# Kernel tuning notes

Hardware: AMD Instinct MI355X
Metric: run time of the kernel (lower is better)

## Reference

```python
import jax, jax.numpy as jnp
import numpy as np

# ---- static config (mirrors init_kwargs) ----
PILLAR_SIZE = 0.075
X_MIN, Y_MIN, Z_MIN = -54.0, -54.0, -5.0
X_MAX, Y_MAX, Z_MAX = 54.0, 54.0, 3.0
GRID_W = int(round((X_MAX - X_MIN) / PILLAR_SIZE))  # 1440
GRID_H = int(round((Y_MAX - Y_MIN) / PILLAR_SIZE))  # 1440
B = 4            # batch (lidar frames)
N = 800_000      # total points across batch
M = 120_000      # total occupied pillars across batch
C_IN = 5         # raw point features (x,y,z,intensity,timestamp)
C_GRP = 6 + C_IN # (xyz - pillar_center, xyz, pt_feature)
C_MLP = 32       # shared MLP output width
BN_EPS = 1e-3


def _pillar_centers(pillar_indices):
    """pillar_indices: (M,3) int [b, y, x] -> (M,3) float centers."""
    pi = pillar_indices.astype(jnp.float32)
    cx = (pi[:, 2] + 0.5) * PILLAR_SIZE + X_MIN
    cy = (pi[:, 1] + 0.5) * PILLAR_SIZE + Y_MIN
    cz = jnp.full_like(cx, 0.5 * (Z_MIN + Z_MAX))
    return jnp.stack([cx, cy, cz], axis=1)


def setup_inputs() -> dict:
    key = jax.random.key(0)
    ks = jax.random.split(key, 8)
    # occupied pillar cells [b, y, x]
    pil_b = jax.random.randint(ks[0], (M,), 0, B, dtype=jnp.int32)
    pil_y = jax.random.randint(ks[1], (M,), 0, GRID_H, dtype=jnp.int32)
    pil_x = jax.random.randint(ks[2], (M,), 0, GRID_W, dtype=jnp.int32)
    pillar_indices = jnp.stack([pil_b, pil_y, pil_x], axis=1)
    # each point belongs to exactly one pillar
    pillar_set_indices = jax.random.randint(ks[3], (N,), 0, M, dtype=jnp.int32)
    centers = _pillar_centers(pillar_indices)
    noise = jax.random.normal(ks[4], (N, 3), dtype=jnp.float32)
    noise = noise * jnp.array([0.3 * PILLAR_SIZE, 0.3 * PILLAR_SIZE, 1.5], jnp.float32)
    xyz = centers[pillar_set_indices] + noise  # points near their pillar center
    pt_feature = jax.random.normal(ks[5], (N, C_IN), dtype=jnp.float32)
    # shared MLP params: Linear(no bias) + BatchNorm1d(gamma, beta)
    W1 = jax.random.normal(ks[6], (C_GRP, C_MLP), dtype=jnp.float32) * np.float32(1.0 / np.sqrt(C_GRP))
    gamma1 = jnp.ones((C_MLP,), jnp.float32)
    beta1 = jnp.zeros((C_MLP,), jnp.float32)
    xyz_batch_cnt = jnp.full((B,), N // B, jnp.int32)
    return dict(xyz=xyz, pt_feature=pt_feature, W1=W1, gamma1=gamma1, beta1=beta1,
                pillar_indices=pillar_indices, pillar_set_indices=pillar_set_indices,
                xyz_batch_cnt=xyz_batch_cnt)


def reference(xyz, pt_feature, W1, gamma1, beta1, pillar_indices, pillar_set_indices, xyz_batch_cnt):
    # --- PillarQueryAndGroup: gather per-point grouped features ---
    centers = _pillar_centers(pillar_indices)            # (M, 3)
    ctr = centers[pillar_set_indices]                    # (N, 3) gather
    group_features = jnp.concatenate([xyz - ctr, xyz, pt_feature], axis=1)  # (N, 6+C)
    # --- shared MLP: Linear(no bias) -> BatchNorm1d (train-mode stats) -> ReLU ---
    h = group_features @ W1                              # (N, C_MLP)
    mean = jnp.mean(h, axis=0)
    var = jnp.var(h, axis=0)                             # biased, as torch BN uses for normalization
    h = (h - mean) * jax.lax.rsqrt(var + BN_EPS) * gamma1 + beta1
    h = jax.nn.relu(h)
    # --- scatter-max pool over pillars (CUDA scatter_max inits to 0) ---
    pooled = jax.ops.segment_max(h, pillar_set_indices, num_segments=M)
    pillar_features = jnp.maximum(pooled, 0.0)           # empty pillars -> 0; h >= 0 after ReLU
    return pillar_features                               # (M, C_MLP); dense features of SparseConvTensor
```

## Files before the change

kernel.cpp:

```cpp
#include <hip/hip_runtime.h>


#define CMLP 32
#define BN_EPS 1e-3f
#define PSIZE 0.075f
#define XMIN -54.0f
#define YMIN -54.0f
#define CZ   -1.0f
#define NREP 64
#define SCATB 4096

__device__ __forceinline__ unsigned enc_f(float x) {
  unsigned b = __float_as_uint(x);
  return (b & 0x80000000u) ? ~b : (b | 0x80000000u);
}
__device__ __forceinline__ float dec_f(unsigned u) {
  unsigned b = (u & 0x80000000u) ? (u & 0x7fffffffu) : ~u;
  return __uint_as_float(b);
}

__global__ void __launch_bounds__(256) scatter_stats_kernel(
    const float* __restrict__ xyz, const float* __restrict__ ptf,
    const float* __restrict__ W1, const float* __restrict__ gamma,
    const int* __restrict__ pil, const int* __restrict__ sidx,
    float* __restrict__ stats_rep, unsigned* __restrict__ outenc, int N) {
  const int tid = threadIdx.x;
  const int c = tid & 31;
  const float w0 = W1[0 * CMLP + c], w1 = W1[1 * CMLP + c];
  const float w2 = W1[2 * CMLP + c];
  const float wx = w0 + W1[3 * CMLP + c];
  const float wy = w1 + W1[4 * CMLP + c];
  const float wz = w2 + W1[5 * CMLP + c];
  const float nw0 = -w0, nw1 = -w1;
  const float c0 = -CZ * w2;
  const float w6 = W1[6 * CMLP + c], w7 = W1[7 * CMLP + c];
  const float w8 = W1[8 * CMLP + c], w9 = W1[9 * CMLP + c];
  const float w10 = W1[10 * CMLP + c];
  const float sgn = (gamma[c] < 0.f) ? -1.f : 1.f;
  float s = 0.f, ss = 0.f;
  const int hw0 = (blockIdx.x * 256 + tid) >> 5;
  const int nhw = (SCATB * 256) >> 5;
  int p = hw0;
  int m = (p < N) ? __builtin_nontemporal_load(&sidx[p]) : 0;
  while (p < N) {
    const int pn = p + nhw;
    const int mn = (pn < N) ? __builtin_nontemporal_load(&sidx[pn]) : 0;
    float cx = fmaf((float)pil[3 * m + 2] + 0.5f, PSIZE, XMIN);
    float cy = fmaf((float)pil[3 * m + 1] + 0.5f, PSIZE, YMIN);
    float x = __builtin_nontemporal_load(&xyz[3 * p]);
    float y = __builtin_nontemporal_load(&xyz[3 * p + 1]);
    float z = __builtin_nontemporal_load(&xyz[3 * p + 2]);
    float h = c0;
    h = fmaf(x, wx, h);
    h = fmaf(y, wy, h);
    h = fmaf(z, wz, h);
    h = fmaf(cx, nw0, h);
    h = fmaf(cy, nw1, h);
    h = fmaf(__builtin_nontemporal_load(&ptf[5 * p + 0]), w6, h);
    h = fmaf(__builtin_nontemporal_load(&ptf[5 * p + 1]), w7, h);
    h = fmaf(__builtin_nontemporal_load(&ptf[5 * p + 2]), w8, h);
    h = fmaf(__builtin_nontemporal_load(&ptf[5 * p + 3]), w9, h);
    h = fmaf(__builtin_nontemporal_load(&ptf[5 * p + 4]), w10, h);
    s += h;
    ss = fmaf(h, h, ss);
    atomicMax(&outenc[m * CMLP + c], enc_f(sgn * h));
    p = pn;
    m = mn;
  }
  s += __shfl_xor(s, 32);
  ss += __shfl_xor(ss, 32);
  __shared__ float red[4][64];
  const int wave = tid >> 6, lane = tid & 63;
  if (lane < 32) {
    red[wave][lane] = s;
    red[wave][32 + lane] = ss;
  }
  __syncthreads();
  if (tid < 64) {
    float v = red[0][tid] + red[1][tid] + red[2][tid] + red[3][tid];
    atomicAdd(&stats_rep[(blockIdx.x & (NREP - 1)) * 64 + tid], v);
  }
}

__global__ void finalize_kernel(const float* __restrict__ gamma,
                                const float* __restrict__ beta,
                                const float* __restrict__ stats_rep,
                                float* __restrict__ affine, float invN) {
  int c = threadIdx.x;
  if (c < CMLP) {
    float s = 0.f, ss = 0.f;
    for (int r = 0; r < NREP; r++) {
      s += stats_rep[r * 64 + c];
      ss += stats_rep[r * 64 + 32 + c];
    }
    float mean = s * invN;
    float var = ss * invN - mean * mean;
    float sc = gamma[c] * rsqrtf(var + BN_EPS);
    affine[c] = sc;
    affine[CMLP + c] = beta[c] - mean * sc;
  }
}

__global__ void __launch_bounds__(256) transform_kernel(
    unsigned* __restrict__ io, const float* __restrict__ affine, int total) {
  int i = blockIdx.x * 256 + threadIdx.x;
  if (i < total) {
    unsigned u = io[i];
    int c = i & 31;
    float v = 0.f;
    if (u) v = fmaxf(fmaf(fabsf(affine[c]), dec_f(u), affine[CMLP + c]), 0.f);
    io[i] = __float_as_uint(v);
  }
}

extern "C" void kernel_launch(void* const* d_in, const int* in_sizes, int n_in,
                              void* d_out, int out_size, void* d_ws, size_t ws_size,
                              hipStream_t stream) {
  const float* xyz = (const float*)d_in[0];
  const float* ptf = (const float*)d_in[1];
  const float* W1 = (const float*)d_in[2];
  const float* gamma = (const float*)d_in[3];
  const float* beta = (const float*)d_in[4];
  const int* pil = (const int*)d_in[5];
  const int* sidx = (const int*)d_in[6];
  unsigned* out = (unsigned*)d_out;

  int N = in_sizes[0] / 3;

  float* stats_rep = (float*)d_ws;
  float* affine = (float*)((char*)d_ws + NREP * 64 * sizeof(float));

  hipMemsetAsync(stats_rep, 0, NREP * 64 * sizeof(float), stream);
  hipMemsetAsync(out, 0, (size_t)out_size * sizeof(unsigned), stream);

  scatter_stats_kernel<<<SCATB, 256, 0, stream>>>(xyz, ptf, W1, gamma, pil,
                                                  sidx, stats_rep, out, N);
  finalize_kernel<<<1, 64, 0, stream>>>(gamma, beta, stats_rep, affine,
                                        1.0f / (float)N);
  transform_kernel<<<(out_size + 255) / 256, 256, 0, stream>>>(out, affine,
                                                               out_size);
}
```

Measured before the change: 189.3 us.

## Bucket points by pillar group and pool in shared memory instead of global atomics

Adds a counting-sort pipeline: a histogram of points per 32-pillar bucket, a prefix scan, and a scatter of point records into bucket order. A pool kernel then computes the MLP output per bucket and reduces the max with LDS atomics, writing each output tile once. This replaces scattered global atomicMax traffic and the output memset, at the cost of extra passes that write and re-read about 36 bytes per point through workspace. The fallback path, used when the workspace is too small, drops the nontemporal loads and adds a read-before-atomicMax check.

```diff
diff --git a/kernel.cpp b/kernel.cpp
--- a/kernel.cpp
+++ b/kernel.cpp
@@ -9,6 +9,9 @@
 #define CZ   -1.0f
 #define NREP 64
 #define SCATB 4096
+#define PPB 32
+#define HISTB 1024
+#define SCAT2B 2048
 
 __device__ __forceinline__ unsigned enc_f(float x) {
   unsigned b = __float_as_uint(x);
@@ -17,6 +20,136 @@
 __device__ __forceinline__ float dec_f(unsigned u) {
   unsigned b = (u & 0x80000000u) ? (u & 0x7fffffffu) : ~u;
   return __uint_as_float(b);
+}
+
+__global__ void __launch_bounds__(256) hist_kernel(
+    const int* __restrict__ sidx, int* __restrict__ hist, int N) {
+  const int stride = gridDim.x * 256;
+  for (int p = blockIdx.x * 256 + threadIdx.x; p < N; p += stride) {
+    int m = __builtin_nontemporal_load(&sidx[p]);
+    atomicAdd(&hist[m >> 5], 1);
+  }
+}
+
+__global__ void prefix_kernel(const int* __restrict__ hist,
+                              int* __restrict__ offs, int* __restrict__ cur,
+                              int nbkt) {
+  __shared__ int part[257];
+  const int t = threadIdx.x;
+  const int chunk = (nbkt + 255) >> 8;
+  const int lo = t * chunk;
+  const int hi = (lo + chunk < nbkt) ? lo + chunk : nbkt;
+  int s = 0;
+  for (int i = lo; i < hi; i++) s += hist[i];
+  part[t] = s;
+  __syncthreads();
+  if (t == 0) {
+    int acc = 0;
+    for (int i = 0; i < 256; i++) { int v = part[i]; part[i] = acc; acc += v; }
+    part[256] = acc;
+  }
+  __syncthreads();
+  int acc = part[t];
+  for (int i = lo; i < hi; i++) {
+    offs[i] = acc;
+    cur[i] = acc;
+    acc += hist[i];
+  }
+  if (t == 0) offs[nbkt] = part[256];
+}
+
+__global__ void __launch_bounds__(256) bucket_scatter_kernel(
+    const float* __restrict__ xyz, const float* __restrict__ ptf,
+    const int* __restrict__ sidx, int* __restrict__ cur,
+    float4* __restrict__ recA, float4* __restrict__ recB,
+    float* __restrict__ recC, int N) {
+  const int stride = gridDim.x * 256;
+  for (int p = blockIdx.x * 256 + threadIdx.x; p < N; p += stride) {
+    int m = __builtin_nontemporal_load(&sidx[p]);
+    float x = __builtin_nontemporal_load(&xyz[3 * p]);
+    float y = __builtin_nontemporal_load(&xyz[3 * p + 1]);
+    float z = __builtin_nontemporal_load(&xyz[3 * p + 2]);
+    float f0 = __builtin_nontemporal_load(&ptf[5 * p + 0]);
+    float f1 = __builtin_nontemporal_load(&ptf[5 * p + 1]);
+    float f2 = __builtin_nontemporal_load(&ptf[5 * p + 2]);
+    float f3 = __builtin_nontemporal_load(&ptf[5 * p + 3]);
+    float f4 = __builtin_nontemporal_load(&ptf[5 * p + 4]);
+    int idx = atomicAdd(&cur[m >> 5], 1);
+    recA[idx] = make_float4(x, y, z, __int_as_float(m));
+    recB[idx] = make_float4(f0, f1, f2, f3);
+    recC[idx] = f4;
+  }
+}
+
+__global__ void __launch_bounds__(256) pool_kernel(
+    const float4* __restrict__ recA, const float4* __restrict__ recB,
+    const float* __restrict__ recC, const int* __restrict__ offs,
+    const float* __restrict__ W1, const float* __restrict__ gamma,
+    const int* __restrict__ pil, float* __restrict__ stats_rep,
+    unsigned* __restrict__ outenc, int M) {
+  __shared__ unsigned lmax[PPB * CMLP];
+  const int tid = threadIdx.x;
+  const int c = tid & 31;
+  for (int i = tid; i < PPB * CMLP; i += 256) lmax[i] = 0u;
+  const float w0 = W1[0 * CMLP + c], w1 = W1[1 * CMLP + c];
+  const float w2 = W1[2 * CMLP + c];
+  const float wx = w0 + W1[3 * CMLP + c];
+  const float wy = w1 + W1[4 * CMLP + c];
+  const float wz = w2 + W1[5 * CMLP + c];
+  const float nw0 = -w0, nw1 = -w1;
+  const float c0 = -CZ * w2;
+  const float w6 = W1[6 * CMLP + c], w7 = W1[7 * CMLP + c];
+  const float w8 = W1[8 * CMLP + c], w9 = W1[9 * CMLP + c];
+  const float w10 = W1[10 * CMLP + c];
+  const float sgn = (gamma[c] < 0.f) ? -1.f : 1.f;
+  const int b = blockIdx.x;
+  const int base = offs[b], end = offs[b + 1];
+  const int p0 = b * PPB;
+  float s = 0.f, ss = 0.f;
+  __syncthreads();
+  for (int i = base + (tid >> 5); i < end; i += 8) {
+    float4 a = recA[i];
+    float4 f = recB[i];
+    float f4 = recC[i];
+    int m = __float_as_int(a.w);
+    float cx = fmaf((float)pil[3 * m + 2] + 0.5f, PSIZE, XMIN);
+    float cy = fmaf((float)pil[3 * m + 1] + 0.5f, PSIZE, YMIN);
+    float h = c0;
+    h = fmaf(a.x, wx, h);
+    h = fmaf(a.y, wy, h);
+    h = fmaf(a.z, wz, h);
+    h = fmaf(cx, nw0, h);
+    h = fmaf(cy, nw1, h);
+    h = fmaf(f.x, w6, h);
+    h = fmaf(f.y, w7, h);
+    h = fmaf(f.z, w8, h);
+    h = fmaf(f.w, w9, h);
+    h = fmaf(f4, w10, h);
+    s += h;
+    ss = fmaf(h, h, ss);
+    atomicMax(&lmax[((m - p0) << 5) | c], enc_f(sgn * h));
+  }
+  __syncthreads();
+  const int gbase = b * (PPB * CMLP);
+  const int glim = M * CMLP;
+#pragma unroll
+  for (int k = 0; k < 4; k++) {
+    int g = gbase + tid + k * 256;
+    if (g < glim) outenc[g] = lmax[tid + k * 256];
+  }
+  s += __shfl_xor(s, 32);
+  ss += __shfl_xor(ss, 32);
+  __shared__ float red[4][64];
+  const int wave = tid >> 6, lane = tid & 63;
+  if (lane < 32) {
+    red[wave][lane] = s;
+    red[wave][32 + lane] = ss;
+  }
+  __syncthreads();
+  if (tid < 64) {
+    float v = red[0][tid] + red[1][tid] + red[2][tid] + red[3][tid];
+    atomicAdd(&stats_rep[(blockIdx.x & (NREP - 1)) * 64 + tid], v);
+  }
 }
 
 __global__ void __launch_bounds__(256) scatter_stats_kernel(
@@ -41,29 +174,29 @@
   const int hw0 = (blockIdx.x * 256 + tid) >> 5;
   const int nhw = (SCATB * 256) >> 5;
   int p = hw0;
-  int m = (p < N) ? __builtin_nontemporal_load(&sidx[p]) : 0;
+  int m = (p < N) ? sidx[p] : 0;
   while (p < N) {
     const int pn = p + nhw;
-    const int mn = (pn < N) ? __builtin_nontemporal_load(&sidx[pn]) : 0;
+    const int mn = (pn < N) ? sidx[pn] : 0;
     float cx = fmaf((float)pil[3 * m + 2] + 0.5f, PSIZE, XMIN);
     float cy = fmaf((float)pil[3 * m + 1] + 0.5f, PSIZE, YMIN);
-    float x = __builtin_nontemporal_load(&xyz[3 * p]);
-    float y = __builtin_nontemporal_load(&xyz[3 * p + 1]);
-    float z = __builtin_nontemporal_load(&xyz[3 * p + 2]);
+    float x = xyz[3 * p], y = xyz[3 * p + 1], z = xyz[3 * p + 2];
     float h = c0;
     h = fmaf(x, wx, h);
     h = fmaf(y, wy, h);
     h = fmaf(z, wz, h);
     h = fmaf(cx, nw0, h);
     h = fmaf(cy, nw1, h);
-    h = fmaf(__builtin_nontemporal_load(&ptf[5 * p + 0]), w6, h);
-    h = fmaf(__builtin_nontemporal_load(&ptf[5 * p + 1]), w7, h);
-    h = fmaf(__builtin_nontemporal_load(&ptf[5 * p + 2]), w8, h);
-    h = fmaf(__builtin_nontemporal_load(&ptf[5 * p + 3]), w9, h);
-    h = fmaf(__builtin_nontemporal_load(&ptf[5 * p + 4]), w10, h);
+    h = fmaf(ptf[5 * p + 0], w6, h);
+    h = fmaf(ptf[5 * p + 1], w7, h);
+    h = fmaf(ptf[5 * p + 2], w8, h);
+    h = fmaf(ptf[5 * p + 3], w9, h);
+    h = fmaf(ptf[5 * p + 4], w10, h);
     s += h;
     ss = fmaf(h, h, ss);
-    atomicMax(&outenc[m * CMLP + c], enc_f(sgn * h));
+    unsigned u = enc_f(sgn * h);
+    unsigned* addr = &outenc[m * CMLP + c];
+    if (u > *addr) atomicMax(addr, u);
     p = pn;
     m = mn;
   }
@@ -126,15 +259,35 @@
   unsigned* out = (unsigned*)d_out;
 
   int N = in_sizes[0] / 3;
-
-  float* stats_rep = (float*)d_ws;
-  float* affine = (float*)((char*)d_ws + NREP * 64 * sizeof(float));
+  int M = out_size / CMLP;
+  int nbkt = (M + PPB - 1) / PPB;
+
+  char* w = (char*)d_ws;
+  float* stats_rep = (float*)w;                 size_t off = NREP * 64 * sizeof(float);
+  float* affine = (float*)(w + off);            off += 64 * sizeof(float);
+  int* hist = (int*)(w + off);                  off += (size_t)nbkt * sizeof(int);
+  int* offs = (int*)(w + off);                  off += (size_t)(nbkt + 1) * sizeof(int);
+  int* cur = (int*)(w + off);                   off += (size_t)nbkt * sizeof(int);
+  off = (off + 15) & ~(size_t)15;
+  float4* recA = (float4*)(w + off);            off += (size_t)N * sizeof(float4);
+  float4* recB = (float4*)(w + off);            off += (size_t)N * sizeof(float4);
+  float* recC = (float*)(w + off);              off += (size_t)N * sizeof(float);
 
   hipMemsetAsync(stats_rep, 0, NREP * 64 * sizeof(float), stream);
-  hipMemsetAsync(out, 0, (size_t)out_size * sizeof(unsigned), stream);
-
-  scatter_stats_kernel<<<SCATB, 256, 0, stream>>>(xyz, ptf, W1, gamma, pil,
-                                                  sidx, stats_rep, out, N);
+
+  if (ws_size >= off) {
+    hipMemsetAsync(hist, 0, (size_t)nbkt * sizeof(int), stream);
+    hist_kernel<<<HISTB, 256, 0, stream>>>(sidx, hist, N);
+    prefix_kernel<<<1, 256, 0, stream>>>(hist, offs, cur, nbkt);
+    bucket_scatter_kernel<<<SCAT2B, 256, 0, stream>>>(xyz, ptf, sidx, cur,
+                                                      recA, recB, recC, N);
+    pool_kernel<<<nbkt, 256, 0, stream>>>(recA, recB, recC, offs, W1, gamma,
+                                          pil, stats_rep, out, M);
+  } else {
+    hipMemsetAsync(out, 0, (size_t)out_size * sizeof(unsigned), stream);
+    scatter_stats_kernel<<<SCATB, 256, 0, stream>>>(xyz, ptf, W1, gamma, pil,
+                                                    sidx, stats_rep, out, N);
+  }
   finalize_kernel<<<1, 64, 0, stream>>>(gamma, beta, stats_rep, affine,
                                         1.0f / (float)N);
   transform_kernel<<<(out_size + 255) / 256, 256, 0, stream>>>(out, affine,
```

After: 286.0 us. 51.1% more time.

## Software-pipeline point loads one iteration ahead and skip redundant atomicMax

Applied to the files above, without the earlier changes.

Each thread now prefetches the next point's index, pillar coordinates, xyz, features and the current encoded output value one iteration ahead, so gather latency overlaps the current point's compute. It also reads the destination's current max early and issues atomicMax only when the new encoded value exceeds the prefetched one, cutting atomic traffic. The prefetched value may be stale, but the atomic still guarantees correctness. The cost is higher register pressure and an extra load per point.

```diff
diff --git a/kernel.cpp b/kernel.cpp
--- a/kernel.cpp
+++ b/kernel.cpp
@@ -40,32 +40,67 @@
   float s = 0.f, ss = 0.f;
   const int hw0 = (blockIdx.x * 256 + tid) >> 5;
   const int nhw = (SCATB * 256) >> 5;
+
   int p = hw0;
-  int m = (p < N) ? __builtin_nontemporal_load(&sidx[p]) : 0;
+  int m = 0, py = 0, px = 0;
+  float x = 0.f, y = 0.f, z = 0.f, f0 = 0.f, f1 = 0.f, f2 = 0.f, f3 = 0.f,
+        f4 = 0.f;
+  unsigned uf = 0xffffffffu;
+  if (p < N) {
+    m = __builtin_nontemporal_load(&sidx[p]);
+    py = pil[3 * m + 1];
+    px = pil[3 * m + 2];
+    x = __builtin_nontemporal_load(&xyz[3 * p]);
+    y = __builtin_nontemporal_load(&xyz[3 * p + 1]);
+    z = __builtin_nontemporal_load(&xyz[3 * p + 2]);
+    f0 = __builtin_nontemporal_load(&ptf[5 * p + 0]);
+    f1 = __builtin_nontemporal_load(&ptf[5 * p + 1]);
+    f2 = __builtin_nontemporal_load(&ptf[5 * p + 2]);
+    f3 = __builtin_nontemporal_load(&ptf[5 * p + 3]);
+    f4 = __builtin_nontemporal_load(&ptf[5 * p + 4]);
+    uf = outenc[m * CMLP + c];
+  }
   while (p < N) {
     const int pn = p + nhw;
-    const int mn = (pn < N) ? __builtin_nontemporal_load(&sidx[pn]) : 0;
-    float cx = fmaf((float)pil[3 * m + 2] + 0.5f, PSIZE, XMIN);
-    float cy = fmaf((float)pil[3 * m + 1] + 0.5f, PSIZE, YMIN);
-    float x = __builtin_nontemporal_load(&xyz[3 * p]);
-    float y = __builtin_nontemporal_load(&xyz[3 * p + 1]);
-    float z = __builtin_nontemporal_load(&xyz[3 * p + 2]);
+    int mn = 0, pyn = 0, pxn = 0;
+    float xn = 0.f, yn = 0.f, zn = 0.f, g0 = 0.f, g1 = 0.f, g2 = 0.f,
+          g3 = 0.f, g4 = 0.f;
+    unsigned ufn = 0xffffffffu;
+    if (pn < N) {
+      mn = __builtin_nontemporal_load(&sidx[pn]);
+      pyn = pil[3 * mn + 1];
+      pxn = pil[3 * mn + 2];
+      xn = __builtin_nontemporal_load(&xyz[3 * pn]);
+      yn = __builtin_nontemporal_load(&xyz[3 * pn + 1]);
+      zn = __builtin_nontemporal_load(&xyz[3 * pn + 2]);
+      g0 = __builtin_nontemporal_load(&ptf[5 * pn + 0]);
+      g1 = __builtin_nontemporal_load(&ptf[5 * pn + 1]);
+      g2 = __builtin_nontemporal_load(&ptf[5 * pn + 2]);
+      g3 = __builtin_nontemporal_load(&ptf[5 * pn + 3]);
+      g4 = __builtin_nontemporal_load(&ptf[5 * pn + 4]);
+      ufn = outenc[mn * CMLP + c];
+    }
+    float cx = fmaf((float)px + 0.5f, PSIZE, XMIN);
+    float cy = fmaf((float)py + 0.5f, PSIZE, YMIN);
     float h = c0;
     h = fmaf(x, wx, h);
     h = fmaf(y, wy, h);
     h = fmaf(z, wz, h);
     h = fmaf(cx, nw0, h);
     h = fmaf(cy, nw1, h);
-    h = fmaf(__builtin_nontemporal_load(&ptf[5 * p + 0]), w6, h);
-    h = fmaf(__builtin_nontemporal_load(&ptf[5 * p + 1]), w7, h);
-    h = fmaf(__builtin_nontemporal_load(&ptf[5 * p + 2]), w8, h);
-    h = fmaf(__builtin_nontemporal_load(&ptf[5 * p + 3]), w9, h);
-    h = fmaf(__builtin_nontemporal_load(&ptf[5 * p + 4]), w10, h);
+    h = fmaf(f0, w6, h);
+    h = fmaf(f1, w7, h);
+    h = fmaf(f2, w8, h);
+    h = fmaf(f3, w9, h);
+    h = fmaf(f4, w10, h);
     s += h;
     ss = fmaf(h, h, ss);
-    atomicMax(&outenc[m * CMLP + c], enc_f(sgn * h));
-    p = pn;
-    m = mn;
+    unsigned u = enc_f(sgn * h);
+    if (u > uf) atomicMax(&outenc[m * CMLP + c], u);
+    p = pn; m = mn; py = pyn; px = pxn;
+    x = xn; y = yn; z = zn;
+    f0 = g0; f1 = g1; f2 = g2; f3 = g3; f4 = g4;
+    uf = ufn;
   }
   s += __shfl_xor(s, 32);
   ss += __shfl_xor(ss, 32);
```

Result: faster. 185.2 us (-2.2%).

## Pack per-pillar max into fp16 pairs updated by 32-bit CAS

Applied to the files above, without the earlier changes.

Encodes the pre-BN activation as an order-preserving 16-bit half and packs two channels per 32-bit word. Even lanes merge their own value and their partner lane's value into the word with an atomicCAS loop, which halves the number of atomic operations and the size of the scatter buffer. The transform kernel then decodes both halves and writes float2 outputs. This costs fp16 rounding of the max values, which may break tolerance, and CAS retries under contention, and each iteration adds a plain read before the CAS.

```diff
diff --git a/kernel.cpp b/kernel.cpp
--- a/kernel.cpp
+++ b/kernel.cpp
@@ -1,4 +1,5 @@
 #include <hip/hip_runtime.h>
+#include <hip/hip_fp16.h>
 
 
 #define CMLP 32
@@ -10,20 +11,24 @@
 #define NREP 64
 #define SCATB 4096
 
-__device__ __forceinline__ unsigned enc_f(float x) {
-  unsigned b = __float_as_uint(x);
-  return (b & 0x80000000u) ? ~b : (b | 0x80000000u);
+__device__ __forceinline__ unsigned enc16(float x) {
+  unsigned short b = __half_as_ushort(__float2half(x));
+  unsigned short e = (b & 0x8000) ? (unsigned short)~b
+                                  : (unsigned short)(b | 0x8000);
+  return (unsigned)e;
 }
-__device__ __forceinline__ float dec_f(unsigned u) {
-  unsigned b = (u & 0x80000000u) ? (u & 0x7fffffffu) : ~u;
-  return __uint_as_float(b);
+__device__ __forceinline__ float dec16(unsigned u) {
+  unsigned short e = (unsigned short)u;
+  unsigned short b = (e & 0x8000) ? (unsigned short)(e & 0x7FFF)
+                                  : (unsigned short)~e;
+  return __half2float(__ushort_as_half(b));
 }
 
 __global__ void __launch_bounds__(256) scatter_stats_kernel(
     const float* __restrict__ xyz, const float* __restrict__ ptf,
     const float* __restrict__ W1, const float* __restrict__ gamma,
     const int* __restrict__ pil, const int* __restrict__ sidx,
-    float* __restrict__ stats_rep, unsigned* __restrict__ outenc, int N) {
+    float* __restrict__ stats_rep, unsigned* __restrict__ out16w, int N) {
   const int tid = threadIdx.x;
   const int c = tid & 31;
   const float w0 = W1[0 * CMLP + c], w1 = W1[1 * CMLP + c];
@@ -63,7 +68,23 @@
     h = fmaf(__builtin_nontemporal_load(&ptf[5 * p + 4]), w10, h);
     s += h;
     ss = fmaf(h, h, ss);
-    atomicMax(&outenc[m * CMLP + c], enc_f(sgn * h));
+    unsigned e = enc16(sgn * h);
+    unsigned partner = (unsigned)__shfl_xor((int)e, 1);
+    if ((c & 1) == 0) {
+      unsigned* addr = &out16w[m * (CMLP / 2) + (c >> 1)];
+      unsigned cur = *addr;
+      unsigned lo = e > (cur & 0xFFFFu) ? e : (cur & 0xFFFFu);
+      unsigned hi = partner > (cur >> 16) ? partner : (cur >> 16);
+      unsigned des = lo | (hi << 16);
+      while (des != cur) {
+        unsigned old = atomicCAS(addr, cur, des);
+        if (old == cur) break;
+        cur = old;
+        lo = e > (cur & 0xFFFFu) ? e : (cur & 0xFFFFu);
+        hi = partner > (cur >> 16) ? partner : (cur >> 16);
+        des = lo | (hi << 16);
+      }
+    }
     p = pn;
     m = mn;
   }
@@ -102,14 +123,17 @@
 }
 
 __global__ void __launch_bounds__(256) transform_kernel(
-    unsigned* __restrict__ io, const float* __restrict__ affine, int total) {
-  int i = blockIdx.x * 256 + threadIdx.x;
-  if (i < total) {
-    unsigned u = io[i];
-    int c = i & 31;
-    float v = 0.f;
-    if (u) v = fmaxf(fmaf(fabsf(affine[c]), dec_f(u), affine[CMLP + c]), 0.f);
-    io[i] = __float_as_uint(v);
+    const unsigned* __restrict__ in16w, const float* __restrict__ affine,
+    float2* __restrict__ out2, int nwords) {
+  int w = blockIdx.x * 256 + threadIdx.x;
+  if (w < nwords) {
+    unsigned u = in16w[w];
+    int c0 = (w << 1) & 31;
+    float v0 = 0.f, v1 = 0.f;
+    unsigned lo = u & 0xFFFFu, hi = u >> 16;
+    if (lo) v0 = fmaxf(fmaf(fabsf(affine[c0]), dec16(lo), affine[CMLP + c0]), 0.f);
+    if (hi) v1 = fmaxf(fmaf(fabsf(affine[c0 + 1]), dec16(hi), affine[CMLP + c0 + 1]), 0.f);
+    out2[w] = make_float2(v0, v1);
   }
 }
 
@@ -123,20 +147,22 @@
   const float* beta = (const float*)d_in[4];
   const int* pil = (const int*)d_in[5];
   const int* sidx = (const int*)d_in[6];
-  unsigned* out = (unsigned*)d_out;
 
   int N = in_sizes[0] / 3;
+  int nwords = out_size / 2;
 
-  float* stats_rep = (float*)d_ws;
-  float* affine = (float*)((char*)d_ws + NREP * 64 * sizeof(float));
+  char* wsp = (char*)d_ws;
+  float* stats_rep = (float*)wsp;
+  float* affine = (float*)(wsp + NREP * 64 * sizeof(float));
+  unsigned* out16w = (unsigned*)(wsp + NREP * 64 * sizeof(float) + 256);
 
   hipMemsetAsync(stats_rep, 0, NREP * 64 * sizeof(float), stream);
-  hipMemsetAsync(out, 0, (size_t)out_size * sizeof(unsigned), stream);
+  hipMemsetAsync(out16w, 0, (size_t)nwords * sizeof(unsigned), stream);
 
   scatter_stats_kernel<<<SCATB, 256, 0, stream>>>(xyz, ptf, W1, gamma, pil,
-                                                  sidx, stats_rep, out, N);
+                                                  sidx, stats_rep, out16w, N);
   finalize_kernel<<<1, 64, 0, stream>>>(gamma, beta, stats_rep, affine,
                                         1.0f / (float)N);
-  transform_kernel<<<(out_size + 255) / 256, 256, 0, stream>>>(out, affine,
-                                                               out_size);
+  transform_kernel<<<(nwords + 255) / 256, 256, 0, stream>>>(
+      out16w, affine, (float2*)d_out, nwords);
 }
```

Result: slower. 199.7 us (+5.5%).
